# Optimization experiments

Measured on AMD Instinct MI355X. Metric: run time of the kernel, lower is better.

The kernel has to match this reference:

```python
import jax, jax.numpy as jnp
import numpy as np

K = 20
EPS = 1e-5
DIMS = [(8, 64), (64, 64), (64, 128), (128, 256), (256, 512), (512, 1024)]
EMB = 512


def edge_conv(x, W, gamma, beta):
    # x: [B, C, N]; W: [O, 2C]
    xt = jnp.swapaxes(x, 1, 2)                      # [B, N, C]
    inner = -2.0 * jnp.einsum('bnc,bmc->bnm', xt, xt)
    xx = jnp.sum(xt * xt, axis=-1)                  # [B, N]
    pd = -xx[:, :, None] - inner - xx[:, None, :]   # -||xi-xj||^2
    idx = jax.lax.top_k(pd, K)[1]                   # [B, N, K]
    nbr = jax.vmap(lambda f, i: f[i])(xt, idx)      # [B, N, K, C] gather
    ctr = xt[:, :, None, :]
    edge = jnp.concatenate([nbr - ctr, jnp.broadcast_to(ctr, nbr.shape)], axis=-1)  # [B,N,K,2C]
    h = jnp.einsum('bnkc,oc->bnko', edge, W)        # 1x1 conv
    mean = jnp.mean(h, axis=(0, 1, 2))
    var = jnp.var(h, axis=(0, 1, 2))
    h = (h - mean) * jax.lax.rsqrt(var + EPS) * gamma + beta  # BatchNorm2d (train stats)
    h = jnp.where(h > 0, h, 0.2 * h)                # LeakyReLU(0.2)
    return jnp.transpose(jnp.max(h, axis=2), (0, 2, 1))  # max over k -> [B, O, N]


def setup_inputs() -> dict:
    key = jax.random.key(0)
    ks = jax.random.split(key, 32)
    d = {"x": jax.random.normal(ks[0], (4, 8, 1024), dtype=jnp.float32)}
    for i, (cin, cout) in enumerate(DIMS):
        fan_in = 2 * cin
        std = float(np.sqrt(2.0 / ((1.0 + 0.2 ** 2) * fan_in)))
        d[f"W{i+1}"] = jax.random.normal(ks[1 + i], (cout, 2 * cin), dtype=jnp.float32) * std
        d[f"g{i+1}"] = jnp.ones((cout,), dtype=jnp.float32)
        d[f"b{i+1}"] = jnp.zeros((cout,), dtype=jnp.float32)
    d["Wm"] = jax.random.normal(ks[20], (EMB, 4096), dtype=jnp.float32) * float(1.0 / np.sqrt(4096))
    d["bm"] = jnp.zeros((EMB,), dtype=jnp.float32)
    d["gm"] = jnp.ones((EMB,), dtype=jnp.float32)
    d["betam"] = jnp.zeros((EMB,), dtype=jnp.float32)
    return d


def reference(x, W1, g1, b1, W2, g2, b2, W3, g3, b3, W4, g4, b4,
              W5, g5, b5, W6, g6, b6, Wm, bm, gm, betam):
    x1 = edge_conv(x, W1, g1, b1)
    x2 = edge_conv(x1, W2, g2, b2)
    x3 = edge_conv(x2, W3, g3, b3)
    x4 = edge_conv(x3, W4, g4, b4)
    x5 = edge_conv(x4, W5, g5, b5)
    x6 = edge_conv(x5, W6, g6, b6)
    feat = jnp.concatenate([x1, x2, x3, x4, x5, x6], axis=1)  # [B, 2048, N]
    p1 = jnp.max(feat, axis=-1)
    p2 = jnp.mean(feat, axis=-1)
    z = jnp.concatenate([p1, p2], axis=1) @ Wm.T + bm         # [B, 4096] -> [B, EMB]
    mean = jnp.mean(z, axis=0)
    var = jnp.var(z, axis=0)
    z = (z - mean) * jax.lax.rsqrt(var + EPS) * gm + betam    # BatchNorm1d
    return jnp.where(z > 0, z, 0.2 * z)
```

## Files before the change

### kernel.cpp

```cpp
#include <hip/hip_runtime.h>
#include <math.h>

#define BATCH 4
#define NPTS 1024
#define KNN 20
#define EPS 1e-5f
#define FEATC 2048
#define KC 16


__global__ __launch_bounds__(256, 2)
void gram_kernel(const float* __restrict__ x, int Cin, size_t bstride,
                 float* __restrict__ G, float* __restrict__ xx) {
    int b = blockIdx.z;
    int n0 = blockIdx.y * 64;
    int m0 = blockIdx.x * 128;
    const float* xb = x + (size_t)b * bstride;
    __shared__ float As[KC][64];
    __shared__ float Bs[KC][128];
    int tid = threadIdx.x;
    int tn = tid % 16, tm = tid / 16;
    float acc[4][8] = {};

    const int ia = tid * 4, cca = ia >> 6, nna = ia & 63;
    const int ib = tid * 8, ccb = ib >> 7, mmb = ib & 127;
    float4 pa, pb0, pb1;
    auto prefetch = [&](int c0) {
        pa = make_float4(0.f, 0.f, 0.f, 0.f);
        pb0 = make_float4(0.f, 0.f, 0.f, 0.f);
        pb1 = make_float4(0.f, 0.f, 0.f, 0.f);
        if (c0 + cca < Cin) pa = *(const float4*)(xb + (size_t)(c0 + cca) * NPTS + n0 + nna);
        if (c0 + ccb < Cin) {
            const float* r = xb + (size_t)(c0 + ccb) * NPTS + m0 + mmb;
            pb0 = *(const float4*)(r);
            pb1 = *(const float4*)(r + 4);
        }
    };
    prefetch(0);
    for (int c0 = 0; c0 < Cin; c0 += KC) {
        *(float4*)(&As[cca][nna]) = pa;
        *(float4*)(&Bs[ccb][mmb]) = pb0;
        *(float4*)(&Bs[ccb][mmb + 4]) = pb1;
        __syncthreads();
        if (c0 + KC < Cin) prefetch(c0 + KC);
#pragma unroll
        for (int cc = 0; cc < KC; ++cc) {
            float4 a4 = *(const float4*)(&As[cc][tn * 4]);
            float4 b0 = *(const float4*)(&Bs[cc][tm * 8]);
            float4 b1 = *(const float4*)(&Bs[cc][tm * 8 + 4]);
            float a[4] = {a4.x, a4.y, a4.z, a4.w};
            float bb[8] = {b0.x, b0.y, b0.z, b0.w, b1.x, b1.y, b1.z, b1.w};
#pragma unroll
            for (int i = 0; i < 4; i++)
#pragma unroll
                for (int j = 0; j < 8; j++) acc[i][j] += a[i] * bb[j];
        }
        __syncthreads();
    }
    float* Gb = G + (size_t)b * NPTS * NPTS;
#pragma unroll
    for (int i = 0; i < 4; i++) {
        int n = n0 + tn * 4 + i;
        size_t row = (size_t)n * NPTS + m0 + tm * 8;
        *(float4*)(Gb + row)     = make_float4(acc[i][0], acc[i][1], acc[i][2], acc[i][3]);
        *(float4*)(Gb + row + 4) = make_float4(acc[i][4], acc[i][5], acc[i][6], acc[i][7]);
#pragma unroll
        for (int j = 0; j < 8; j++)
            if (n == m0 + tm * 8 + j) xx[b * NPTS + n] = acc[i][j];
    }
}

__global__ __launch_bounds__(256)
void topk_kernel(const float* __restrict__ G, const float* __restrict__ xx,
                 int* __restrict__ idx) {
    int wid = threadIdx.x >> 6, lane = threadIdx.x & 63;
    int t = blockIdx.x * 4 + wid;
    int b = t >> 10, n = t & (NPTS - 1);
    const float* Gr = G + ((size_t)b * NPTS + n) * NPTS;
    const float* xxb = xx + b * NPTS;
    float xxn = xxb[n];
    float d[16];
    int base = lane * 4;
#pragma unroll
    for (int c = 0; c < 4; ++c) {
        float4 gv = *(const float4*)(Gr + c * 256 + base);
        float4 xv = *(const float4*)(xxb + c * 256 + base);
        d[c * 4 + 0] = (2.f * gv.x - xxn) - xv.x;
        d[c * 4 + 1] = (2.f * gv.y - xxn) - xv.y;
        d[c * 4 + 2] = (2.f * gv.z - xxn) - xv.z;
        d[c * 4 + 3] = (2.f * gv.w - xxn) - xv.w;
    }
    int* out = idx + (size_t)t * KNN;
    for (int k = 0; k < KNN; ++k) {
        float bv = d[0]; int bs = 0;
#pragma unroll
        for (int s = 1; s < 16; ++s)
            if (d[s] > bv) { bv = d[s]; bs = s; }
        int bm = ((bs >> 2) << 8) + base + (bs & 3);
#pragma unroll
        for (int off = 32; off >= 1; off >>= 1) {
            float ov = __shfl_xor(bv, off);
            int om = __shfl_xor(bm, off);
            if (ov > bv || (ov == bv && om < bm)) { bv = ov; bm = om; }
        }
        if (lane == 0) out[k] = bm;
        int rel = bm - base;
#pragma unroll
        for (int s = 0; s < 16; ++s)
            if (rel == (((s >> 2) << 8) | (s & 3))) d[s] = -INFINITY;
    }
}

__global__ __launch_bounds__(256, 2)
void pq_gemm_kernel(const float* __restrict__ x, int Cin, size_t bstride,
                    const float* __restrict__ W, int Cout,
                    float* __restrict__ p, float* __restrict__ q) {
    int b = blockIdx.z;
    int o0 = blockIdx.x * 64;
    int n0 = blockIdx.y * 64;
    const float* xb = x + (size_t)b * bstride;
    __shared__ float W1s[KC][64];
    __shared__ float WQs[KC][64];
    __shared__ float Xs[KC][64];
    int tid = threadIdx.x;
    int tn = tid % 16;
    int tm = tid / 16;
    float accp[4][4] = {};
    float accq[4][4] = {};

    const int ix = tid * 4, ccx = ix >> 6, nnx = ix & 63;
    const int r = tid % 64, cg = (tid / 64) * 4;
    const float* Wr = W + (size_t)(o0 + r) * 2 * Cin;
    float4 px, pw1, pw2;
    auto prefetch = [&](int c0) {
        px = make_float4(0.f, 0.f, 0.f, 0.f);
        pw1 = make_float4(0.f, 0.f, 0.f, 0.f);
        pw2 = make_float4(0.f, 0.f, 0.f, 0.f);
        if (c0 + ccx < Cin) px = *(const float4*)(xb + (size_t)(c0 + ccx) * NPTS + n0 + nnx);
        if (c0 + cg < Cin) {
            pw1 = *(const float4*)(Wr + c0 + cg);
            pw2 = *(const float4*)(Wr + Cin + c0 + cg);
        }
    };
    prefetch(0);
    for (int c0 = 0; c0 < Cin; c0 += KC) {
        *(float4*)(&Xs[ccx][nnx]) = px;
        W1s[cg + 0][r] = pw1.x; WQs[cg + 0][r] = pw2.x - pw1.x;
        W1s[cg + 1][r] = pw1.y; WQs[cg + 1][r] = pw2.y - pw1.y;
        W1s[cg + 2][r] = pw1.z; WQs[cg + 2][r] = pw2.z - pw1.z;
        W1s[cg + 3][r] = pw1.w; WQs[cg + 3][r] = pw2.w - pw1.w;
        __syncthreads();
        if (c0 + KC < Cin) prefetch(c0 + KC);
#pragma unroll
        for (int cc = 0; cc < KC; ++cc) {
            float4 wv = *(const float4*)(&W1s[cc][tn * 4]);
            float4 qv = *(const float4*)(&WQs[cc][tn * 4]);
            float4 xv = *(const float4*)(&Xs[cc][tm * 4]);
            float w1[4] = {wv.x, wv.y, wv.z, wv.w};
            float wq[4] = {qv.x, qv.y, qv.z, qv.w};
            float xj[4] = {xv.x, xv.y, xv.z, xv.w};
#pragma unroll
            for (int i = 0; i < 4; i++)
#pragma unroll
                for (int j = 0; j < 4; j++) {
                    accp[i][j] += w1[i] * xj[j];
                    accq[i][j] += wq[i] * xj[j];
                }
        }
        __syncthreads();
    }
#pragma unroll
    for (int j = 0; j < 4; j++) {
        int n = n0 + tm * 4 + j;
        size_t base = ((size_t)b * NPTS + n) * Cout + o0 + tn * 4;
        *(float4*)(p + base) = make_float4(accp[0][j], accp[1][j], accp[2][j], accp[3][j]);
        *(float4*)(q + base) = make_float4(accq[0][j], accq[1][j], accq[2][j], accq[3][j]);
    }
}

__global__ __launch_bounds__(256, 2)
void pq_n128_kernel(const float* __restrict__ x, int Cin, size_t bstride,
                    const float* __restrict__ W, int Cout,
                    float* __restrict__ p, float* __restrict__ q) {
    int b = blockIdx.z;
    int o0 = blockIdx.x * 64;
    int n0 = blockIdx.y * 128;
    const float* xb = x + (size_t)b * bstride;
    __shared__ float W1s[KC][64];
    __shared__ float WQs[KC][64];
    __shared__ float Xs[KC][128];
    int tid = threadIdx.x;
    int tn = tid % 16;
    int tm = tid / 16;
    float accp[4][8] = {};
    float accq[4][8] = {};

    const int ccx = tid / 16, nnx = (tid * 8) & 127;
    const int r = tid % 64, cg = (tid / 64) * 4;
    const float* Wr = W + (size_t)(o0 + r) * 2 * Cin;
    float4 px0, px1, pw1, pw2;
    auto prefetch = [&](int c0) {
        px0 = make_float4(0.f, 0.f, 0.f, 0.f);
        px1 = make_float4(0.f, 0.f, 0.f, 0.f);
        pw1 = make_float4(0.f, 0.f, 0.f, 0.f);
        pw2 = make_float4(0.f, 0.f, 0.f, 0.f);
        if (c0 + ccx < Cin) {
            const float* rx = xb + (size_t)(c0 + ccx) * NPTS + n0 + nnx;
            px0 = *(const float4*)(rx);
            px1 = *(const float4*)(rx + 4);
        }
        if (c0 + cg < Cin) {
            pw1 = *(const float4*)(Wr + c0 + cg);
            pw2 = *(const float4*)(Wr + Cin + c0 + cg);
        }
    };
    prefetch(0);
    for (int c0 = 0; c0 < Cin; c0 += KC) {
        *(float4*)(&Xs[ccx][nnx]) = px0;
        *(float4*)(&Xs[ccx][nnx + 4]) = px1;
        W1s[cg + 0][r] = pw1.x; WQs[cg + 0][r] = pw2.x - pw1.x;
        W1s[cg + 1][r] = pw1.y; WQs[cg + 1][r] = pw2.y - pw1.y;
        W1s[cg + 2][r] = pw1.z; WQs[cg + 2][r] = pw2.z - pw1.z;
        W1s[cg + 3][r] = pw1.w; WQs[cg + 3][r] = pw2.w - pw1.w;
        __syncthreads();
        if (c0 + KC < Cin) prefetch(c0 + KC);
#pragma unroll
        for (int cc = 0; cc < KC; ++cc) {
            float4 wv = *(const float4*)(&W1s[cc][tn * 4]);
            float4 qv = *(const float4*)(&WQs[cc][tn * 4]);
            float4 x0 = *(const float4*)(&Xs[cc][tm * 4]);
            float4 x1 = *(const float4*)(&Xs[cc][64 + tm * 4]);
            float w1[4] = {wv.x, wv.y, wv.z, wv.w};
            float wq[4] = {qv.x, qv.y, qv.z, qv.w};
            float xj[8] = {x0.x, x0.y, x0.z, x0.w, x1.x, x1.y, x1.z, x1.w};
#pragma unroll
            for (int i = 0; i < 4; i++)
#pragma unroll
                for (int j = 0; j < 8; j++) {
                    accp[i][j] += w1[i] * xj[j];
                    accq[i][j] += wq[i] * xj[j];
                }
        }
        __syncthreads();
    }
#pragma unroll
    for (int j = 0; j < 4; j++) {
        int n = n0 + tm * 4 + j;
        size_t base = ((size_t)b * NPTS + n) * Cout + o0 + tn * 4;
        *(float4*)(p + base) = make_float4(accp[0][j], accp[1][j], accp[2][j], accp[3][j]);
        *(float4*)(q + base) = make_float4(accq[0][j], accq[1][j], accq[2][j], accq[3][j]);
    }
#pragma unroll
    for (int j = 0; j < 4; j++) {
        int n = n0 + 64 + tm * 4 + j;
        size_t base = ((size_t)b * NPTS + n) * Cout + o0 + tn * 4;
        *(float4*)(p + base) = make_float4(accp[0][j + 4], accp[1][j + 4], accp[2][j + 4], accp[3][j + 4]);
        *(float4*)(q + base) = make_float4(accq[0][j + 4], accq[1][j + 4], accq[2][j + 4], accq[3][j + 4]);
    }
}

template <int COUT>
__global__ void stats_kernel(const float* __restrict__ p, const float* __restrict__ q,
                             const int* __restrict__ idx,
                             float* __restrict__ partials) {
    constexpr int CA = (COUT < 256) ? COUT : 256;
    constexpr int NCH = COUT / CA;
    constexpr int CV = CA / 4;
    constexpr int PP = 256 / CV;
    constexpr int NCHUNK = 16;
    int bid = blockIdx.x;
    int b = bid / (NPTS / NCHUNK);
    int n0 = (bid % (NPTS / NCHUNK)) * NCHUNK;
    int cl = threadIdx.x % CV;
    int sub = threadIdx.x / CV;
    int c = blockIdx.y * CA + cl * 4;
    float sx = 0.f, sy = 0.f, sz = 0.f, sw = 0.f;
    float tx = 0.f, ty = 0.f, tz = 0.f, tw = 0.f;
    for (int nl = sub; nl < NCHUNK; nl += PP) {
        size_t nb = (size_t)b * NPTS + n0 + nl;
        const int* ixp = idx + nb * KNN;
        float4 qv = *(const float4*)(q + nb * COUT + c);
        for (int k = 0; k < KNN; ++k) {
            int m = ixp[k];
            float4 pv = *(const float4*)(p + ((size_t)b * NPTS + m) * COUT + c);
            float vx = pv.x + qv.x, vy = pv.y + qv.y, vz = pv.z + qv.z, vw = pv.w + qv.w;
            sx += vx; sy += vy; sz += vz; sw += vw;
            tx += vx * vx; ty += vy * vy; tz += vz * vz; tw += vw * vw;
        }
    }
    __shared__ float4 red[256];
    red[threadIdx.x] = make_float4(sx, sy, sz, sw);
    __syncthreads();
    for (int st = PP / 2; st > 0; st >>= 1) {
        if (sub < st) {
            float4 o = red[threadIdx.x + st * CV];
            float4 m = red[threadIdx.x];
            red[threadIdx.x] = make_float4(m.x + o.x, m.y + o.y, m.z + o.z, m.w + o.w);
        }
        __syncthreads();
    }
    if (sub == 0) { float4 m = red[cl]; sx = m.x; sy = m.y; sz = m.z; sw = m.w; }
    __syncthreads();
    red[threadIdx.x] = make_float4(tx, ty, tz, tw);
    __syncthreads();
    for (int st = PP / 2; st > 0; st >>= 1) {
        if (sub < st) {
            float4 o = red[threadIdx.x + st * CV];
            float4 m = red[threadIdx.x];
            red[threadIdx.x] = make_float4(m.x + o.x, m.y + o.y, m.z + o.z, m.w + o.w);
        }
        __syncthreads();
    }
    if (sub == 0) {
        float4 m = red[cl];
        float* outp = partials + ((size_t)bid * NCH + blockIdx.y) * 2 * CA;
        *(float4*)(outp + cl * 4) = make_float4(sx, sy, sz, sw);
        *(float4*)(outp + CA + cl * 4) = m;
    }
}

__global__ void scaleshift_kernel(const float* __restrict__ partials, const float* __restrict__ g,
                                  const float* __restrict__ beta, int Cout, int nblk,
                                  int CA, int NCH, float* __restrict__ sc) {
    int c = blockIdx.x * 256 + threadIdx.x;
    if (c >= Cout) return;
    int chunk = c / CA, within = c % CA;
    float s0 = 0.f, s1 = 0.f;
    for (int b = 0; b < nblk; ++b) {
        const float* pp = partials + ((size_t)b * NCH + chunk) * 2 * CA;
        s0 += pp[within];
        s1 += pp[CA + within];
    }
    float cnt = (float)(BATCH * NPTS * KNN);
    float mean = s0 / cnt;
    float var = s1 / cnt - mean * mean;
    float s = g[c] * rsqrtf(var + EPS);
    sc[c] = s;
    sc[Cout + c] = beta[c] - mean * s;
}

__global__ void apply_kernel(const float* __restrict__ p, const float* __restrict__ q,
                             const int* __restrict__ idx, const float* __restrict__ sc,
                             int Cout, int choff, float* __restrict__ feat) {
    __shared__ float tile[32][33];
    __shared__ int nidx[32][KNN];
    int b = blockIdx.z;
    int c0 = blockIdx.x * 32, n0 = blockIdx.y * 32;
    int tid = threadIdx.x;
    for (int i = tid; i < 32 * KNN; i += 256) {
        int nn = i / KNN, kk = i % KNN;
        nidx[nn][kk] = idx[((size_t)b * NPTS + n0 + nn) * KNN + kk];
    }
    __syncthreads();
    int tx4 = tid % 8, ny = tid / 8;
    int c = c0 + tx4 * 4;
    float4 s4 = *(const float4*)(sc + c);
    float4 sh4 = *(const float4*)(sc + Cout + c);
    size_t nb = (size_t)b * NPTS + n0 + ny;
    float4 qv = *(const float4*)(q + nb * Cout + c);
    float mx[4] = {-INFINITY, -INFINITY, -INFINITY, -INFINITY};
    float mn[4] = {INFINITY, INFINITY, INFINITY, INFINITY};
    for (int k = 0; k < KNN; ++k) {
        int m = nidx[ny][k];
        float4 pv = *(const float4*)(p + ((size_t)b * NPTS + m) * Cout + c);
        float v0 = pv.x + qv.x, v1 = pv.y + qv.y, v2 = pv.z + qv.z, v3 = pv.w + qv.w;
        mx[0] = fmaxf(mx[0], v0); mn[0] = fminf(mn[0], v0);
        mx[1] = fmaxf(mx[1], v1); mn[1] = fminf(mn[1], v1);
        mx[2] = fmaxf(mx[2], v2); mn[2] = fminf(mn[2], v2);
        mx[3] = fmaxf(mx[3], v3); mn[3] = fminf(mn[3], v3);
    }
    float sa[4] = {s4.x, s4.y, s4.z, s4.w};
    float sha[4] = {sh4.x, sh4.y, sh4.z, sh4.w};
#pragma unroll
    for (int u = 0; u < 4; u++) {
        float v = (sa[u] >= 0.f) ? mx[u] : mn[u];
        v = sa[u] * v + sha[u];
        tile[ny][tx4 * 4 + u] = (v > 0.f) ? v : 0.2f * v;
    }
    __syncthreads();
    int wtx = tid % 32, wty = tid / 32;
    for (int i = wty; i < 32; i += 8) {
        feat[((size_t)b * FEATC + choff + c0 + i) * NPTS + n0 + wtx] = tile[wtx][i];
    }
}

__global__ void pool_kernel(const float* __restrict__ feat, float* __restrict__ pooled) {
    int t = blockIdx.x;
    int b = t >> 11, c = t & (FEATC - 1);
    const float* row = feat + (size_t)t * NPTS;
    int tid = threadIdx.x;
    float mx = -INFINITY, sm = 0.f;
    for (int n = tid; n < NPTS; n += 256) { float v = row[n]; mx = fmaxf(mx, v); sm += v; }
    __shared__ float smx[256], ssm[256];
    smx[tid] = mx; ssm[tid] = sm;
    __syncthreads();
    for (int s = 128; s > 0; s >>= 1) {
        if (tid < s) { smx[tid] = fmaxf(smx[tid], smx[tid + s]); ssm[tid] += ssm[tid + s]; }
        __syncthreads();
    }
    if (tid == 0) {
        pooled[b * 4096 + c] = smx[0];
        pooled[b * 4096 + 2048 + c] = ssm[0] * (1.f / NPTS);
    }
}

__global__ void final_kernel(const float* __restrict__ pooled, const float* __restrict__ Wm,
                             const float* __restrict__ bm, const float* __restrict__ gm,
                             const float* __restrict__ betam, float* __restrict__ out) {
    int o = blockIdx.x;
    int tid = threadIdx.x;
    float acc[BATCH] = {};
    for (int t = tid; t < 4096; t += 256) {
        float w = Wm[(size_t)o * 4096 + t];
#pragma unroll
        for (int b = 0; b < BATCH; b++) acc[b] += w * pooled[b * 4096 + t];
    }
    __shared__ float red[256];
    float zb[BATCH];
    for (int b = 0; b < BATCH; b++) {
        red[tid] = acc[b];
        __syncthreads();
        for (int s = 128; s > 0; s >>= 1) {
            if (tid < s) red[tid] += red[tid + s];
            __syncthreads();
        }
        zb[b] = red[0];
        __syncthreads();
    }
    if (tid == 0) {
        float z[BATCH];
        float mean = 0.f;
        for (int b = 0; b < BATCH; b++) { z[b] = zb[b] + bm[o]; mean += z[b]; }
        mean *= (1.f / BATCH);
        float var = 0.f;
        for (int b = 0; b < BATCH; b++) { float d = z[b] - mean; var += d * d; }
        var *= (1.f / BATCH);
        float s = gm[o] * rsqrtf(var + EPS);
        for (int b = 0; b < BATCH; b++) {
            float v = (z[b] - mean) * s + betam[o];
            out[b * 512 + o] = (v > 0.f) ? v : 0.2f * v;
        }
    }
}

extern "C" void kernel_launch(void* const* d_in, const int* in_sizes, int n_in,
                              void* d_out, int out_size, void* d_ws, size_t ws_size,
                              hipStream_t stream) {
    const float* x = (const float*)d_in[0];
    const float* Wm = (const float*)d_in[19];
    const float* bm = (const float*)d_in[20];
    const float* gm = (const float*)d_in[21];
    const float* betam = (const float*)d_in[22];
    float* out = (float*)d_out;

    char* ws = (char*)d_ws;
    float* G        = (float*)(ws);
    float* p        = G;
    float* q        = (float*)(ws + (size_t)(16 << 20));
    float* feat     = (float*)(ws + (size_t)(32 << 20));
    int*   idx      = (int*)  (ws + (size_t)(64 << 20));
    float* xx       = (float*)(ws + (size_t)(64 << 20) + (384 << 10));
    float* sc       = (float*)(ws + (size_t)(64 << 20) + (448 << 10));
    float* pooled   = (float*)(ws + (size_t)(64 << 20) + (512 << 10));
    float* partials = (float*)(ws + (size_t)(65 << 20));

    const int cins[6]   = {8, 64, 64, 128, 256, 512};
    const int couts[6]  = {64, 64, 128, 256, 512, 1024};
    const int choffs[6] = {0, 64, 128, 256, 512, 1024};

    const float* xin = x;
    size_t bstride = (size_t)8 * NPTS;
    const int NBLK = BATCH * (NPTS / 16);

    for (int L = 0; L < 6; ++L) {
        int Cin = cins[L], Cout = couts[L], choff = choffs[L];
        const float* W = (const float*)d_in[1 + 3 * L];
        const float* g = (const float*)d_in[2 + 3 * L];
        const float* bb = (const float*)d_in[3 + 3 * L];

        gram_kernel<<<dim3(NPTS / 128, NPTS / 64, BATCH), 256, 0, stream>>>(xin, Cin, bstride, G, xx);
        topk_kernel<<<BATCH * NPTS / 4, 256, 0, stream>>>(G, xx, idx);
        if (Cout >= 1024)
            pq_n128_kernel<<<dim3(Cout / 64, NPTS / 128, BATCH), 256, 0, stream>>>(xin, Cin, bstride, W, Cout, p, q);
        else
            pq_gemm_kernel<<<dim3(Cout / 64, NPTS / 64, BATCH), 256, 0, stream>>>(xin, Cin, bstride, W, Cout, p, q);
        int CA = (Cout < 256) ? Cout : 256;
        int NCH = Cout / CA;
        switch (Cout) {
            case 64:   stats_kernel<64>  <<<dim3(NBLK, 1), 256, 0, stream>>>(p, q, idx, partials); break;
            case 128:  stats_kernel<128> <<<dim3(NBLK, 1), 256, 0, stream>>>(p, q, idx, partials); break;
            case 256:  stats_kernel<256> <<<dim3(NBLK, 1), 256, 0, stream>>>(p, q, idx, partials); break;
            case 512:  stats_kernel<512> <<<dim3(NBLK, 2), 256, 0, stream>>>(p, q, idx, partials); break;
            case 1024: stats_kernel<1024><<<dim3(NBLK, 4), 256, 0, stream>>>(p, q, idx, partials); break;
        }
        scaleshift_kernel<<<(Cout + 255) / 256, 256, 0, stream>>>(partials, g, bb, Cout, NBLK, CA, NCH, sc);
        apply_kernel<<<dim3(Cout / 32, NPTS / 32, BATCH), 256, 0, stream>>>(p, q, idx, sc, Cout, choff, feat);

        xin = feat + (size_t)choff * NPTS;
        bstride = (size_t)FEATC * NPTS;
    }

    pool_kernel<<<BATCH * FEATC, 256, 0, stream>>>(feat, pooled);
    final_kernel<<<512, 256, 0, stream>>>(pooled, Wm, bm, gm, betam, out);
}
```

Measured before the change: 1.063 ms.

## Fuse Gram and PQ GEMMs into one launch with relocated p buffer

Merges the per-layer Gram-matrix GEMM and the p/q projection GEMM into a single launch. Block indices below a threshold compute the Gram tile and the rest compute the projection tile, so the two independent GEMMs share the GPU instead of running back to back. Because p previously aliased the Gram buffer, p moves into the unused upper half of each batch slot of the feature buffer. The last layer's output is redirected into the freed Gram buffer, and the pooling kernel reads those channels from there. This cuts one launch per layer and aims to improve occupancy on the small layers, at the cost of more complex workspace aliasing and a larger shared-memory footprint for the Gram blocks.

After: 1.061 ms. No clear change (-0.2%).

```diff
diff --git a/kernel.cpp b/kernel.cpp
--- a/kernel.cpp
+++ b/kernel.cpp
@@ -7,66 +7,209 @@
 #define EPS 1e-5f
 #define FEATC 2048
 #define KC 16
-
-
+#define PQ_BSTRIDE 2097152
+
+
+template <bool PQN128>
 __global__ __launch_bounds__(256, 2)
-void gram_kernel(const float* __restrict__ x, int Cin, size_t bstride,
-                 float* __restrict__ G, float* __restrict__ xx) {
+void grampq_kernel(const float* __restrict__ x, int Cin, size_t bstride,
+                   const float* __restrict__ W, int Cout,
+                   float* __restrict__ G, float* __restrict__ xx,
+                   float* __restrict__ pB, float* __restrict__ q,
+                   int ngram, int npqo) {
+    __shared__ float smem[KC * 256];
     int b = blockIdx.z;
-    int n0 = blockIdx.y * 64;
-    int m0 = blockIdx.x * 128;
     const float* xb = x + (size_t)b * bstride;
-    __shared__ float As[KC][64];
-    __shared__ float Bs[KC][128];
     int tid = threadIdx.x;
     int tn = tid % 16, tm = tid / 16;
-    float acc[4][8] = {};
-
-    const int ia = tid * 4, cca = ia >> 6, nna = ia & 63;
-    const int ib = tid * 8, ccb = ib >> 7, mmb = ib & 127;
-    float4 pa, pb0, pb1;
-    auto prefetch = [&](int c0) {
-        pa = make_float4(0.f, 0.f, 0.f, 0.f);
-        pb0 = make_float4(0.f, 0.f, 0.f, 0.f);
-        pb1 = make_float4(0.f, 0.f, 0.f, 0.f);
-        if (c0 + cca < Cin) pa = *(const float4*)(xb + (size_t)(c0 + cca) * NPTS + n0 + nna);
-        if (c0 + ccb < Cin) {
-            const float* r = xb + (size_t)(c0 + ccb) * NPTS + m0 + mmb;
-            pb0 = *(const float4*)(r);
-            pb1 = *(const float4*)(r + 4);
-        }
-    };
-    prefetch(0);
-    for (int c0 = 0; c0 < Cin; c0 += KC) {
-        *(float4*)(&As[cca][nna]) = pa;
-        *(float4*)(&Bs[ccb][mmb]) = pb0;
-        *(float4*)(&Bs[ccb][mmb + 4]) = pb1;
-        __syncthreads();
-        if (c0 + KC < Cin) prefetch(c0 + KC);
-#pragma unroll
-        for (int cc = 0; cc < KC; ++cc) {
-            float4 a4 = *(const float4*)(&As[cc][tn * 4]);
-            float4 b0 = *(const float4*)(&Bs[cc][tm * 8]);
-            float4 b1 = *(const float4*)(&Bs[cc][tm * 8 + 4]);
-            float a[4] = {a4.x, a4.y, a4.z, a4.w};
-            float bb[8] = {b0.x, b0.y, b0.z, b0.w, b1.x, b1.y, b1.z, b1.w};
-#pragma unroll
-            for (int i = 0; i < 4; i++)
-#pragma unroll
-                for (int j = 0; j < 8; j++) acc[i][j] += a[i] * bb[j];
-        }
-        __syncthreads();
-    }
-    float* Gb = G + (size_t)b * NPTS * NPTS;
-#pragma unroll
-    for (int i = 0; i < 4; i++) {
-        int n = n0 + tn * 4 + i;
-        size_t row = (size_t)n * NPTS + m0 + tm * 8;
-        *(float4*)(Gb + row)     = make_float4(acc[i][0], acc[i][1], acc[i][2], acc[i][3]);
-        *(float4*)(Gb + row + 4) = make_float4(acc[i][4], acc[i][5], acc[i][6], acc[i][7]);
-#pragma unroll
-        for (int j = 0; j < 8; j++)
-            if (n == m0 + tm * 8 + j) xx[b * NPTS + n] = acc[i][j];
+
+    if ((int)blockIdx.x < ngram) {
+        int bx = blockIdx.x;
+        int m0 = (bx & 7) * 128;
+        int n0 = (bx >> 3) * 64;
+        float (*As)[64] = (float(*)[64])smem;
+        float (*Bs)[128] = (float(*)[128])(smem + KC * 64);
+        float acc[4][8] = {};
+
+        const int ia = tid * 4, cca = ia >> 6, nna = ia & 63;
+        const int ib = tid * 8, ccb = ib >> 7, mmb = ib & 127;
+        float4 pa, pb0, pb1;
+        auto prefetch = [&](int c0) {
+            pa = make_float4(0.f, 0.f, 0.f, 0.f);
+            pb0 = make_float4(0.f, 0.f, 0.f, 0.f);
+            pb1 = make_float4(0.f, 0.f, 0.f, 0.f);
+            if (c0 + cca < Cin) pa = *(const float4*)(xb + (size_t)(c0 + cca) * NPTS + n0 + nna);
+            if (c0 + ccb < Cin) {
+                const float* r = xb + (size_t)(c0 + ccb) * NPTS + m0 + mmb;
+                pb0 = *(const float4*)(r);
+                pb1 = *(const float4*)(r + 4);
+            }
+        };
+        prefetch(0);
+        for (int c0 = 0; c0 < Cin; c0 += KC) {
+            *(float4*)(&As[cca][nna]) = pa;
+            *(float4*)(&Bs[ccb][mmb]) = pb0;
+            *(float4*)(&Bs[ccb][mmb + 4]) = pb1;
+            __syncthreads();
+            if (c0 + KC < Cin) prefetch(c0 + KC);
+#pragma unroll
+            for (int cc = 0; cc < KC; ++cc) {
+                float4 a4 = *(const float4*)(&As[cc][tn * 4]);
+                float4 b0 = *(const float4*)(&Bs[cc][tm * 8]);
+                float4 b1 = *(const float4*)(&Bs[cc][tm * 8 + 4]);
+                float a[4] = {a4.x, a4.y, a4.z, a4.w};
+                float bb[8] = {b0.x, b0.y, b0.z, b0.w, b1.x, b1.y, b1.z, b1.w};
+#pragma unroll
+                for (int i = 0; i < 4; i++)
+#pragma unroll
+                    for (int j = 0; j < 8; j++) acc[i][j] += a[i] * bb[j];
+            }
+            __syncthreads();
+        }
+        float* Gb = G + (size_t)b * NPTS * NPTS;
+#pragma unroll
+        for (int i = 0; i < 4; i++) {
+            int n = n0 + tn * 4 + i;
+            size_t row = (size_t)n * NPTS + m0 + tm * 8;
+            *(float4*)(Gb + row)     = make_float4(acc[i][0], acc[i][1], acc[i][2], acc[i][3]);
+            *(float4*)(Gb + row + 4) = make_float4(acc[i][4], acc[i][5], acc[i][6], acc[i][7]);
+#pragma unroll
+            for (int j = 0; j < 8; j++)
+                if (n == m0 + tm * 8 + j) xx[b * NPTS + n] = acc[i][j];
+        }
+    } else if (!PQN128) {
+        int bx = blockIdx.x - ngram;
+        int o0 = (bx % npqo) * 64;
+        int n0 = (bx / npqo) * 64;
+        float (*W1s)[64] = (float(*)[64])smem;
+        float (*WQs)[64] = (float(*)[64])(smem + KC * 64);
+        float (*Xs)[64]  = (float(*)[64])(smem + KC * 128);
+        float accp[4][4] = {};
+        float accq[4][4] = {};
+
+        const int ix = tid * 4, ccx = ix >> 6, nnx = ix & 63;
+        const int r = tid % 64, cg = (tid / 64) * 4;
+        const float* Wr = W + (size_t)(o0 + r) * 2 * Cin;
+        float4 px, pw1, pw2;
+        auto prefetch = [&](int c0) {
+            px = make_float4(0.f, 0.f, 0.f, 0.f);
+            pw1 = make_float4(0.f, 0.f, 0.f, 0.f);
+            pw2 = make_float4(0.f, 0.f, 0.f, 0.f);
+            if (c0 + ccx < Cin) px = *(const float4*)(xb + (size_t)(c0 + ccx) * NPTS + n0 + nnx);
+            if (c0 + cg < Cin) {
+                pw1 = *(const float4*)(Wr + c0 + cg);
+                pw2 = *(const float4*)(Wr + Cin + c0 + cg);
+            }
+        };
+        prefetch(0);
+        for (int c0 = 0; c0 < Cin; c0 += KC) {
+            *(float4*)(&Xs[ccx][nnx]) = px;
+            W1s[cg + 0][r] = pw1.x; WQs[cg + 0][r] = pw2.x - pw1.x;
+            W1s[cg + 1][r] = pw1.y; WQs[cg + 1][r] = pw2.y - pw1.y;
+            W1s[cg + 2][r] = pw1.z; WQs[cg + 2][r] = pw2.z - pw1.z;
+            W1s[cg + 3][r] = pw1.w; WQs[cg + 3][r] = pw2.w - pw1.w;
+            __syncthreads();
+            if (c0 + KC < Cin) prefetch(c0 + KC);
+#pragma unroll
+            for (int cc = 0; cc < KC; ++cc) {
+                float4 wv = *(const float4*)(&W1s[cc][tn * 4]);
+                float4 qv = *(const float4*)(&WQs[cc][tn * 4]);
+                float4 xv = *(const float4*)(&Xs[cc][tm * 4]);
+                float w1[4] = {wv.x, wv.y, wv.z, wv.w};
+                float wq[4] = {qv.x, qv.y, qv.z, qv.w};
+                float xj[4] = {xv.x, xv.y, xv.z, xv.w};
+#pragma unroll
+                for (int i = 0; i < 4; i++)
+#pragma unroll
+                    for (int j = 0; j < 4; j++) {
+                        accp[i][j] += w1[i] * xj[j];
+                        accq[i][j] += wq[i] * xj[j];
+                    }
+            }
+            __syncthreads();
+        }
+#pragma unroll
+        for (int j = 0; j < 4; j++) {
+            int n = n0 + tm * 4 + j;
+            size_t pbase = (size_t)b * PQ_BSTRIDE + (size_t)n * Cout + o0 + tn * 4;
+            size_t qbase = ((size_t)b * NPTS + n) * Cout + o0 + tn * 4;
+            *(float4*)(pB + pbase) = make_float4(accp[0][j], accp[1][j], accp[2][j], accp[3][j]);
+            *(float4*)(q + qbase) = make_float4(accq[0][j], accq[1][j], accq[2][j], accq[3][j]);
+        }
+    } else {
+        int bx = blockIdx.x - ngram;
+        int o0 = (bx % npqo) * 64;
+        int n0 = (bx / npqo) * 128;
+        float (*W1s)[64]  = (float(*)[64])smem;
+        float (*WQs)[64]  = (float(*)[64])(smem + KC * 64);
+        float (*Xs)[128]  = (float(*)[128])(smem + KC * 128);
+        float accp[4][8] = {};
+        float accq[4][8] = {};
+
+        const int ccx = tid / 16, nnx = (tid * 8) & 127;
+        const int r = tid % 64, cg = (tid / 64) * 4;
+        const float* Wr = W + (size_t)(o0 + r) * 2 * Cin;
+        float4 px0, px1, pw1, pw2;
+        auto prefetch = [&](int c0) {
+            px0 = make_float4(0.f, 0.f, 0.f, 0.f);
+            px1 = make_float4(0.f, 0.f, 0.f, 0.f);
+            pw1 = make_float4(0.f, 0.f, 0.f, 0.f);
+            pw2 = make_float4(0.f, 0.f, 0.f, 0.f);
+            if (c0 + ccx < Cin) {
+                const float* rx = xb + (size_t)(c0 + ccx) * NPTS + n0 + nnx;
+                px0 = *(const float4*)(rx);
+                px1 = *(const float4*)(rx + 4);
+            }
+            if (c0 + cg < Cin) {
+                pw1 = *(const float4*)(Wr + c0 + cg);
+                pw2 = *(const float4*)(Wr + Cin + c0 + cg);
+            }
+        };
+        prefetch(0);
+        for (int c0 = 0; c0 < Cin; c0 += KC) {
+            *(float4*)(&Xs[ccx][nnx]) = px0;
+            *(float4*)(&Xs[ccx][nnx + 4]) = px1;
+            W1s[cg + 0][r] = pw1.x; WQs[cg + 0][r] = pw2.x - pw1.x;
+            W1s[cg + 1][r] = pw1.y; WQs[cg + 1][r] = pw2.y - pw1.y;
+            W1s[cg + 2][r] = pw1.z; WQs[cg + 2][r] = pw2.z - pw1.z;
+            W1s[cg + 3][r] = pw1.w; WQs[cg + 3][r] = pw2.w - pw1.w;
+            __syncthreads();
+            if (c0 + KC < Cin) prefetch(c0 + KC);
+#pragma unroll
+            for (int cc = 0; cc < KC; ++cc) {
+                float4 wv = *(const float4*)(&W1s[cc][tn * 4]);
+                float4 qv = *(const float4*)(&WQs[cc][tn * 4]);
+                float4 x0 = *(const float4*)(&Xs[cc][tm * 4]);
+                float4 x1 = *(const float4*)(&Xs[cc][64 + tm * 4]);
+                float w1[4] = {wv.x, wv.y, wv.z, wv.w};
+                float wq[4] = {qv.x, qv.y, qv.z, qv.w};
+                float xj[8] = {x0.x, x0.y, x0.z, x0.w, x1.x, x1.y, x1.z, x1.w};
+#pragma unroll
+                for (int i = 0; i < 4; i++)
+#pragma unroll
+                    for (int j = 0; j < 8; j++) {
+                        accp[i][j] += w1[i] * xj[j];
+                        accq[i][j] += wq[i] * xj[j];
+                    }
+            }
+            __syncthreads();
+        }
+#pragma unroll
+        for (int j = 0; j < 4; j++) {
+            int n = n0 + tm * 4 + j;
+            size_t pbase = (size_t)b * PQ_BSTRIDE + (size_t)n * Cout + o0 + tn * 4;
+            size_t qbase = ((size_t)b * NPTS + n) * Cout + o0 + tn * 4;
+            *(float4*)(pB + pbase) = make_float4(accp[0][j], accp[1][j], accp[2][j], accp[3][j]);
+            *(float4*)(q + qbase) = make_float4(accq[0][j], accq[1][j], accq[2][j], accq[3][j]);
+        }
+#pragma unroll
+        for (int j = 0; j < 4; j++) {
+            int n = n0 + 64 + tm * 4 + j;
+            size_t pbase = (size_t)b * PQ_BSTRIDE + (size_t)n * Cout + o0 + tn * 4;
+            size_t qbase = ((size_t)b * NPTS + n) * Cout + o0 + tn * 4;
+            *(float4*)(pB + pbase) = make_float4(accp[0][j + 4], accp[1][j + 4], accp[2][j + 4], accp[3][j + 4]);
+            *(float4*)(q + qbase) = make_float4(accq[0][j + 4], accq[1][j + 4], accq[2][j + 4], accq[3][j + 4]);
+        }
     }
 }
 
@@ -111,156 +254,8 @@
     }
 }
 
-__global__ __launch_bounds__(256, 2)
-void pq_gemm_kernel(const float* __restrict__ x, int Cin, size_t bstride,
-                    const float* __restrict__ W, int Cout,
-                    float* __restrict__ p, float* __restrict__ q) {
-    int b = blockIdx.z;
-    int o0 = blockIdx.x * 64;
-    int n0 = blockIdx.y * 64;
-    const float* xb = x + (size_t)b * bstride;
-    __shared__ float W1s[KC][64];
-    __shared__ float WQs[KC][64];
-    __shared__ float Xs[KC][64];
-    int tid = threadIdx.x;
-    int tn = tid % 16;
-    int tm = tid / 16;
-    float accp[4][4] = {};
-    float accq[4][4] = {};
-
-    const int ix = tid * 4, ccx = ix >> 6, nnx = ix & 63;
-    const int r = tid % 64, cg = (tid / 64) * 4;
-    const float* Wr = W + (size_t)(o0 + r) * 2 * Cin;
-    float4 px, pw1, pw2;
-    auto prefetch = [&](int c0) {
-        px = make_float4(0.f, 0.f, 0.f, 0.f);
-        pw1 = make_float4(0.f, 0.f, 0.f, 0.f);
-        pw2 = make_float4(0.f, 0.f, 0.f, 0.f);
-        if (c0 + ccx < Cin) px = *(const float4*)(xb + (size_t)(c0 + ccx) * NPTS + n0 + nnx);
-        if (c0 + cg < Cin) {
-            pw1 = *(const float4*)(Wr + c0 + cg);
-            pw2 = *(const float4*)(Wr + Cin + c0 + cg);
-        }
-    };
-    prefetch(0);
-    for (int c0 = 0; c0 < Cin; c0 += KC) {
-        *(float4*)(&Xs[ccx][nnx]) = px;
-        W1s[cg + 0][r] = pw1.x; WQs[cg + 0][r] = pw2.x - pw1.x;
-        W1s[cg + 1][r] = pw1.y; WQs[cg + 1][r] = pw2.y - pw1.y;
-        W1s[cg + 2][r] = pw1.z; WQs[cg + 2][r] = pw2.z - pw1.z;
-        W1s[cg + 3][r] = pw1.w; WQs[cg + 3][r] = pw2.w - pw1.w;
-        __syncthreads();
-        if (c0 + KC < Cin) prefetch(c0 + KC);
-#pragma unroll
-        for (int cc = 0; cc < KC; ++cc) {
-            float4 wv = *(const float4*)(&W1s[cc][tn * 4]);
-            float4 qv = *(const float4*)(&WQs[cc][tn * 4]);
-            float4 xv = *(const float4*)(&Xs[cc][tm * 4]);
-            float w1[4] = {wv.x, wv.y, wv.z, wv.w};
-            float wq[4] = {qv.x, qv.y, qv.z, qv.w};
-            float xj[4] = {xv.x, xv.y, xv.z, xv.w};
-#pragma unroll
-            for (int i = 0; i < 4; i++)
-#pragma unroll
-                for (int j = 0; j < 4; j++) {
-                    accp[i][j] += w1[i] * xj[j];
-                    accq[i][j] += wq[i] * xj[j];
-                }
-        }
-        __syncthreads();
-    }
-#pragma unroll
-    for (int j = 0; j < 4; j++) {
-        int n = n0 + tm * 4 + j;
-        size_t base = ((size_t)b * NPTS + n) * Cout + o0 + tn * 4;
-        *(float4*)(p + base) = make_float4(accp[0][j], accp[1][j], accp[2][j], accp[3][j]);
-        *(float4*)(q + base) = make_float4(accq[0][j], accq[1][j], accq[2][j], accq[3][j]);
-    }
-}
-
-__global__ __launch_bounds__(256, 2)
-void pq_n128_kernel(const float* __restrict__ x, int Cin, size_t bstride,
-                    const float* __restrict__ W, int Cout,
-                    float* __restrict__ p, float* __restrict__ q) {
-    int b = blockIdx.z;
-    int o0 = blockIdx.x * 64;
-    int n0 = blockIdx.y * 128;
-    const float* xb = x + (size_t)b * bstride;
-    __shared__ float W1s[KC][64];
-    __shared__ float WQs[KC][64];
-    __shared__ float Xs[KC][128];
-    int tid = threadIdx.x;
-    int tn = tid % 16;
-    int tm = tid / 16;
-    float accp[4][8] = {};
-    float accq[4][8] = {};
-
-    const int ccx = tid / 16, nnx = (tid * 8) & 127;
-    const int r = tid % 64, cg = (tid / 64) * 4;
-    const float* Wr = W + (size_t)(o0 + r) * 2 * Cin;
-    float4 px0, px1, pw1, pw2;
-    auto prefetch = [&](int c0) {
-        px0 = make_float4(0.f, 0.f, 0.f, 0.f);
-        px1 = make_float4(0.f, 0.f, 0.f, 0.f);
-        pw1 = make_float4(0.f, 0.f, 0.f, 0.f);
-        pw2 = make_float4(0.f, 0.f, 0.f, 0.f);
-        if (c0 + ccx < Cin) {
-            const float* rx = xb + (size_t)(c0 + ccx) * NPTS + n0 + nnx;
-            px0 = *(const float4*)(rx);
-            px1 = *(const float4*)(rx + 4);
-        }
-        if (c0 + cg < Cin) {
-            pw1 = *(const float4*)(Wr + c0 + cg);
-            pw2 = *(const float4*)(Wr + Cin + c0 + cg);
-        }
-    };
-    prefetch(0);
-    for (int c0 = 0; c0 < Cin; c0 += KC) {
-        *(float4*)(&Xs[ccx][nnx]) = px0;
-        *(float4*)(&Xs[ccx][nnx + 4]) = px1;
-        W1s[cg + 0][r] = pw1.x; WQs[cg + 0][r] = pw2.x - pw1.x;
-        W1s[cg + 1][r] = pw1.y; WQs[cg + 1][r] = pw2.y - pw1.y;
-        W1s[cg + 2][r] = pw1.z; WQs[cg + 2][r] = pw2.z - pw1.z;
-        W1s[cg + 3][r] = pw1.w; WQs[cg + 3][r] = pw2.w - pw1.w;
-        __syncthreads();
-        if (c0 + KC < Cin) prefetch(c0 + KC);
-#pragma unroll
-        for (int cc = 0; cc < KC; ++cc) {
-            float4 wv = *(const float4*)(&W1s[cc][tn * 4]);
-            float4 qv = *(const float4*)(&WQs[cc][tn * 4]);
-            float4 x0 = *(const float4*)(&Xs[cc][tm * 4]);
-            float4 x1 = *(const float4*)(&Xs[cc][64 + tm * 4]);
-            float w1[4] = {wv.x, wv.y, wv.z, wv.w};
-            float wq[4] = {qv.x, qv.y, qv.z, qv.w};
-            float xj[8] = {x0.x, x0.y, x0.z, x0.w, x1.x, x1.y, x1.z, x1.w};
-#pragma unroll
-            for (int i = 0; i < 4; i++)
-#pragma unroll
-                for (int j = 0; j < 8; j++) {
-                    accp[i][j] += w1[i] * xj[j];
-                    accq[i][j] += wq[i] * xj[j];
-                }
-        }
-        __syncthreads();
-    }
-#pragma unroll
-    for (int j = 0; j < 4; j++) {
-        int n = n0 + tm * 4 + j;
-        size_t base = ((size_t)b * NPTS + n) * Cout + o0 + tn * 4;
-        *(float4*)(p + base) = make_float4(accp[0][j], accp[1][j], accp[2][j], accp[3][j]);
-        *(float4*)(q + base) = make_float4(accq[0][j], accq[1][j], accq[2][j], accq[3][j]);
-    }
-#pragma unroll
-    for (int j = 0; j < 4; j++) {
-        int n = n0 + 64 + tm * 4 + j;
-        size_t base = ((size_t)b * NPTS + n) * Cout + o0 + tn * 4;
-        *(float4*)(p + base) = make_float4(accp[0][j + 4], accp[1][j + 4], accp[2][j + 4], accp[3][j + 4]);
-        *(float4*)(q + base) = make_float4(accq[0][j + 4], accq[1][j + 4], accq[2][j + 4], accq[3][j + 4]);
-    }
-}
-
 template <int COUT>
-__global__ void stats_kernel(const float* __restrict__ p, const float* __restrict__ q,
+__global__ void stats_kernel(const float* __restrict__ pB, const float* __restrict__ q,
                              const int* __restrict__ idx,
                              float* __restrict__ partials) {
     constexpr int CA = (COUT < 256) ? COUT : 256;
@@ -274,6 +269,7 @@
     int cl = threadIdx.x % CV;
     int sub = threadIdx.x / CV;
     int c = blockIdx.y * CA + cl * 4;
+    const float* pb = pB + (size_t)b * PQ_BSTRIDE;
     float sx = 0.f, sy = 0.f, sz = 0.f, sw = 0.f;
     float tx = 0.f, ty = 0.f, tz = 0.f, tw = 0.f;
     for (int nl = sub; nl < NCHUNK; nl += PP) {
@@ -282,7 +278,7 @@
         float4 qv = *(const float4*)(q + nb * COUT + c);
         for (int k = 0; k < KNN; ++k) {
             int m = ixp[k];
-            float4 pv = *(const float4*)(p + ((size_t)b * NPTS + m) * COUT + c);
+            float4 pv = *(const float4*)(pb + (size_t)m * COUT + c);
             float vx = pv.x + qv.x, vy = pv.y + qv.y, vz = pv.z + qv.z, vw = pv.w + qv.w;
             sx += vx; sy += vy; sz += vz; sw += vw;
             tx += vx * vx; ty += vy * vy; tz += vz * vz; tw += vw * vw;
@@ -339,9 +335,9 @@
     sc[Cout + c] = beta[c] - mean * s;
 }
 
-__global__ void apply_kernel(const float* __restrict__ p, const float* __restrict__ q,
+__global__ void apply_kernel(const float* __restrict__ pB, const float* __restrict__ q,
                              const int* __restrict__ idx, const float* __restrict__ sc,
-                             int Cout, int choff, float* __restrict__ feat) {
+                             int Cout, int choff, int OC, float* __restrict__ outp) {
     __shared__ float tile[32][33];
     __shared__ int nidx[32][KNN];
     int b = blockIdx.z;
@@ -357,12 +353,13 @@
     float4 s4 = *(const float4*)(sc + c);
     float4 sh4 = *(const float4*)(sc + Cout + c);
     size_t nb = (size_t)b * NPTS + n0 + ny;
+    const float* pb = pB + (size_t)b * PQ_BSTRIDE;
     float4 qv = *(const float4*)(q + nb * Cout + c);
     float mx[4] = {-INFINITY, -INFINITY, -INFINITY, -INFINITY};
     float mn[4] = {INFINITY, INFINITY, INFINITY, INFINITY};
     for (int k = 0; k < KNN; ++k) {
         int m = nidx[ny][k];
-        float4 pv = *(const float4*)(p + ((size_t)b * NPTS + m) * Cout + c);
+        float4 pv = *(const float4*)(pb + (size_t)m * Cout + c);
         float v0 = pv.x + qv.x, v1 = pv.y + qv.y, v2 = pv.z + qv.z, v3 = pv.w + qv.w;
         mx[0] = fmaxf(mx[0], v0); mn[0] = fminf(mn[0], v0);
         mx[1] = fmaxf(mx[1], v1); mn[1] = fminf(mn[1], v1);
@@ -380,14 +377,17 @@
     __syncthreads();
     int wtx = tid % 32, wty = tid / 32;
     for (int i = wty; i < 32; i += 8) {
-        feat[((size_t)b * FEATC + choff + c0 + i) * NPTS + n0 + wtx] = tile[wtx][i];
-    }
-}
-
-__global__ void pool_kernel(const float* __restrict__ feat, float* __restrict__ pooled) {
+        outp[((size_t)b * OC + choff + c0 + i) * NPTS + n0 + wtx] = tile[wtx][i];
+    }
+}
+
+__global__ void pool_kernel(const float* __restrict__ feat, const float* __restrict__ g6,
+                            float* __restrict__ pooled) {
     int t = blockIdx.x;
     int b = t >> 11, c = t & (FEATC - 1);
-    const float* row = feat + (size_t)t * NPTS;
+    const float* row = (c < 1024)
+        ? feat + ((size_t)b * FEATC + c) * NPTS
+        : g6 + ((size_t)b * 1024 + (c - 1024)) * NPTS;
     int tid = threadIdx.x;
     float mx = -INFINITY, sm = 0.f;
     for (int n = tid; n < NPTS; n += 256) { float v = row[n]; mx = fmaxf(mx, v); sm += v; }
@@ -455,7 +455,6 @@
 
     char* ws = (char*)d_ws;
     float* G        = (float*)(ws);
-    float* p        = G;
     float* q        = (float*)(ws + (size_t)(16 << 20));
     float* feat     = (float*)(ws + (size_t)(32 << 20));
     int*   idx      = (int*)  (ws + (size_t)(64 << 20));
@@ -463,6 +462,7 @@
     float* sc       = (float*)(ws + (size_t)(64 << 20) + (448 << 10));
     float* pooled   = (float*)(ws + (size_t)(64 << 20) + (512 << 10));
     float* partials = (float*)(ws + (size_t)(65 << 20));
+    float* pB       = feat + 1048576;
 
     const int cins[6]   = {8, 64, 64, 128, 256, 512};
     const int couts[6]  = {64, 64, 128, 256, 512, 1024};
@@ -471,6 +471,7 @@
     const float* xin = x;
     size_t bstride = (size_t)8 * NPTS;
     const int NBLK = BATCH * (NPTS / 16);
+    const int NGRAM = (NPTS / 128) * (NPTS / 64);
 
     for (int L = 0; L < 6; ++L) {
         int Cin = cins[L], Cout = couts[L], choff = choffs[L];
@@ -478,28 +479,36 @@
         const float* g = (const float*)d_in[2 + 3 * L];
         const float* bb = (const float*)d_in[3 + 3 * L];
 
-        gram_kernel<<<dim3(NPTS / 128, NPTS / 64, BATCH), 256, 0, stream>>>(xin, Cin, bstride, G, xx);
+        int npqo = Cout / 64;
+        if (Cout >= 1024) {
+            int npq = npqo * (NPTS / 128);
+            grampq_kernel<true><<<dim3(NGRAM + npq, 1, BATCH), 256, 0, stream>>>(
+                xin, Cin, bstride, W, Cout, G, xx, pB, q, NGRAM, npqo);
+        } else {
+            int npq = npqo * (NPTS / 64);
+            grampq_kernel<false><<<dim3(NGRAM + npq, 1, BATCH), 256, 0, stream>>>(
+                xin, Cin, bstride, W, Cout, G, xx, pB, q, NGRAM, npqo);
+        }
         topk_kernel<<<BATCH * NPTS / 4, 256, 0, stream>>>(G, xx, idx);
-        if (Cout >= 1024)
-            pq_n128_kernel<<<dim3(Cout / 64, NPTS / 128, BATCH), 256, 0, stream>>>(xin, Cin, bstride, W, Cout, p, q);
-        else
-            pq_gemm_kernel<<<dim3(Cout / 64, NPTS / 64, BATCH), 256, 0, stream>>>(xin, Cin, bstride, W, Cout, p, q);
         int CA = (Cout < 256) ? Cout : 256;
         int NCH = Cout / CA;
         switch (Cout) {
-            case 64:   stats_kernel<64>  <<<dim3(NBLK, 1), 256, 0, stream>>>(p, q, idx, partials); break;
-            case 128:  stats_kernel<128> <<<dim3(NBLK, 1), 256, 0, stream>>>(p, q, idx, partials); break;
-            case 256:  stats_kernel<256> <<<dim3(NBLK, 1), 256, 0, stream>>>(p, q, idx, partials); break;
-            case 512:  stats_kernel<512> <<<dim3(NBLK, 2), 256, 0, stream>>>(p, q, idx, partials); break;
-            case 1024: stats_kernel<1024><<<dim3(NBLK, 4), 256, 0, stream>>>(p, q, idx, partials); break;
+            case 64:   stats_kernel<64>  <<<dim3(NBLK, 1), 256, 0, stream>>>(pB, q, idx, partials); break;
+            case 128:  stats_kernel<128> <<<dim3(NBLK, 1), 256, 0, stream>>>(pB, q, idx, partials); break;
+            case 256:  stats_kernel<256> <<<dim3(NBLK, 1), 256, 0, stream>>>(pB, q, idx, partials); break;
+            case 512:  stats_kernel<512> <<<dim3(NBLK, 2), 256, 0, stream>>>(pB, q, idx, partials); break;
+            case 1024: stats_kernel<1024><<<dim3(NBLK, 4), 256, 0, stream>>>(pB, q, idx, partials); break;
         }
         scaleshift_kernel<<<(Cout + 255) / 256, 256, 0, stream>>>(partials, g, bb, Cout, NBLK, CA, NCH, sc);
-        apply_kernel<<<dim3(Cout / 32, NPTS / 32, BATCH), 256, 0, stream>>>(p, q, idx, sc, Cout, choff, feat);
+        if (L == 5)
+            apply_kernel<<<dim3(Cout / 32, NPTS / 32, BATCH), 256, 0, stream>>>(pB, q, idx, sc, Cout, 0, 1024, G);
+        else
+            apply_kernel<<<dim3(Cout / 32, NPTS / 32, BATCH), 256, 0, stream>>>(pB, q, idx, sc, Cout, choff, FEATC, feat);
 
         xin = feat + (size_t)choff * NPTS;
         bstride = (size_t)FEATC * NPTS;
     }
 
-    pool_kernel<<<BATCH * FEATC, 256, 0, stream>>>(feat, pooled);
+    pool_kernel<<<BATCH * FEATC, 256, 0, stream>>>(feat, G, pooled);
     final_kernel<<<512, 256, 0, stream>>>(pooled, Wm, bm, gm, betam, out);
 }
```
